# Optimization experiments

Hardware: AMD Instinct MI355X
Metric: run time of the kernel (lower is better)

Reference implementation:

```python
import jax, jax.numpy as jnp
import numpy as np

T, B, IN_DIM, HIDDEN = 512, 64, 512, 1024


def setup_inputs() -> dict:
    key = jax.random.key(0)
    k1, k2, k3, k4, k5 = jax.random.split(key, 5)
    x = jax.random.normal(k1, (T, B, IN_DIM), dtype=jnp.float32)
    h0 = jax.random.normal(k2, (B, HIDDEN), dtype=jnp.float32)
    # parameters initialized like torch.rand (uniform [0,1))
    Wx = jax.random.uniform(k3, (IN_DIM, HIDDEN), dtype=jnp.float32)
    Wh = jax.random.uniform(k4, (HIDDEN, HIDDEN), dtype=jnp.float32)
    b = jax.random.uniform(k5, (1, HIDDEN), dtype=jnp.float32)
    return {"x": x, "h0": h0, "Wx": Wx, "Wh": Wh, "b": b}


def reference(x, h0, Wx, Wh, b):
    # Precompute input projections for all timesteps in one big GEMM:
    # [T, B, in_dim] @ [in_dim, hidden] -> [T, B, hidden]
    xw = jnp.einsum('tbi,ih->tbh', x, Wx) + b  # bias fused here

    def step(h, xw_t):
        h = jnp.tanh(xw_t + h @ Wh)
        return h, h

    h_last, outs = jax.lax.scan(step, h0, xw)
    return outs, h_last
```

## Files before the change

kernel.cpp:

```cpp
#include <hip/hip_runtime.h>
#include <hip/hip_bf16.h>


#define T_ 512
#define B_ 64
#define IN_ 512
#define H_ 1024
constexpr int TBH = T_ * B_ * H_;
constexpr int HB  = B_ * H_;
constexpr int GP  = 1024 * 16;

typedef unsigned short u16;
typedef unsigned int u32;
typedef unsigned long long u64;
typedef __attribute__((ext_vector_type(8))) short short8;
typedef __attribute__((ext_vector_type(4))) float f32x4;

__device__ __forceinline__ void splitbf(float x, u16& hi, u16& lo) {
    unsigned u = __float_as_uint(x);
    hi = (u16)(u >> 16);
    float r = x - __uint_as_float(u & 0xffff0000u);
    lo = (u16)(__float_as_uint(r) >> 16);
}

__global__ void k_split4(const float4* __restrict__ in, u16* __restrict__ hi,
                         u16* __restrict__ lo, int n4) {
    int i = blockIdx.x * blockDim.x + threadIdx.x;
    int stride = gridDim.x * blockDim.x;
    for (; i < n4; i += stride) {
        float4 v = in[i];
        u16 h0,h1,h2,h3,l0,l1,l2,l3;
        splitbf(v.x,h0,l0); splitbf(v.y,h1,l1); splitbf(v.z,h2,l2); splitbf(v.w,h3,l3);
        uint2 hv, lv;
        hv.x = (unsigned)h0 | ((unsigned)h1 << 16);
        hv.y = (unsigned)h2 | ((unsigned)h3 << 16);
        lv.x = (unsigned)l0 | ((unsigned)l1 << 16);
        lv.y = (unsigned)l2 | ((unsigned)l3 << 16);
        *(uint2*)&hi[4*i] = hv;
        *(uint2*)&lo[4*i] = lv;
    }
}

__global__ void k_tsplit(const float* __restrict__ src, u16* __restrict__ hi,
                         u16* __restrict__ lo, int K, int N) {
    int id = blockIdx.x * 256 + threadIdx.x;
    if (id >= K * N) return;
    int k = id / N, n = id % N;
    u16 h, l; splitbf(src[id], h, l);
    hi[n*K + k] = h; lo[n*K + k] = l;
}

__global__ void k_h0(const float* __restrict__ h0, u32* __restrict__ hbufP) {
    int id = blockIdx.x * 256 + threadIdx.x;
    if (id >= HB) return;
    int b = id >> 10, k = id & 1023;
    u32 u = __float_as_uint(h0[id]);
    hbufP[(size_t)((b>>4)*2 + 1)*GP + k*16 + (b & 15)] = (u & 0xFFFFFF80u) | 127u;
}

__launch_bounds__(256, 2)
__global__ void k_gemm_xw(const u16* __restrict__ xhi, const u16* __restrict__ xlo,
                          const u16* __restrict__ wthi, const u16* __restrict__ wtlo,
                          const float* __restrict__ bias, float* __restrict__ out) {
    int bid = blockIdx.x;
    int mi = bid >> 3, ni = bid & 7;
    int m0 = mi * 128, n0 = ni * 128;
    int wave = threadIdx.x >> 6, lane = threadIdx.x & 63;
    int wr = wave >> 1, wc = wave & 1;
    int lrow = lane & 15, lk8 = (lane >> 4) * 8;
    const int rowb = m0 + wr*64 + lrow;
    const int colb = n0 + wc*64 + lrow;
    f32x4 acc[4][4] = {};
    for (int kt = 0; kt < 16; ++kt) {
        int kb = kt*32 + lk8;
        short8 ah[4], al[4], bh[4], bl[4];
#pragma unroll
        for (int mt = 0; mt < 4; ++mt) {
            ah[mt] = *(const short8*)&xhi[(size_t)(rowb + mt*16)*IN_ + kb];
            al[mt] = *(const short8*)&xlo[(size_t)(rowb + mt*16)*IN_ + kb];
        }
#pragma unroll
        for (int nt = 0; nt < 4; ++nt) {
            bh[nt] = *(const short8*)&wthi[(size_t)(colb + nt*16)*IN_ + kb];
            bl[nt] = *(const short8*)&wtlo[(size_t)(colb + nt*16)*IN_ + kb];
        }
#pragma unroll
        for (int mt = 0; mt < 4; ++mt)
#pragma unroll
            for (int nt = 0; nt < 4; ++nt) {
                acc[mt][nt] = __builtin_amdgcn_mfma_f32_16x16x32_bf16(ah[mt], bh[nt], acc[mt][nt], 0,0,0);
                acc[mt][nt] = __builtin_amdgcn_mfma_f32_16x16x32_bf16(ah[mt], bl[nt], acc[mt][nt], 0,0,0);
                acc[mt][nt] = __builtin_amdgcn_mfma_f32_16x16x32_bf16(al[mt], bh[nt], acc[mt][nt], 0,0,0);
            }
    }
    int orow0 = m0 + wr*64 + 4*(lane >> 4);
#pragma unroll
    for (int nt = 0; nt < 4; ++nt) {
        int col = n0 + wc*64 + nt*16 + (lane & 15);
        float bv = bias[col];
#pragma unroll
        for (int mt = 0; mt < 4; ++mt)
#pragma unroll
            for (int r = 0; r < 4; ++r)
                out[(size_t)(orow0 + mt*16 + r)*H_ + col] = acc[mt][nt][r] + bv;
    }
}

__global__ void k_gemm_f32(const float* __restrict__ A, const float* __restrict__ Bw,
                           const float* __restrict__ bias, float* __restrict__ out) {
    __shared__ float As[32][65];
    __shared__ float Bs[32][65];
    int n0 = blockIdx.x * 64, m0 = blockIdx.y * 64;
    int tid = threadIdx.x;
    int tr = tid >> 4, tc = tid & 15;
    float acc[4][4] = {};
    for (int kc = 0; kc < IN_; kc += 32) {
#pragma unroll
        for (int it = 0; it < 8; ++it) {
            int id = tid + 256*it;
            int k = id & 31, m = id >> 5;
            As[k][m] = A[(size_t)(m0 + m)*IN_ + kc + k];
        }
#pragma unroll
        for (int it = 0; it < 8; ++it) {
            int id = tid + 256*it;
            int n = id & 63, kk = id >> 6;
            Bs[kk][n] = Bw[(size_t)(kc + kk)*H_ + n0 + n];
        }
        __syncthreads();
#pragma unroll
        for (int kk = 0; kk < 32; ++kk) {
            float a[4], b[4];
#pragma unroll
            for (int i = 0; i < 4; ++i) a[i] = As[kk][tr*4+i];
#pragma unroll
            for (int j = 0; j < 4; ++j) b[j] = Bs[kk][tc*4+j];
#pragma unroll
            for (int i = 0; i < 4; ++i)
#pragma unroll
                for (int j = 0; j < 4; ++j) acc[i][j] += a[i]*b[j];
        }
        __syncthreads();
    }
#pragma unroll
    for (int i = 0; i < 4; ++i)
#pragma unroll
        for (int j = 0; j < 4; ++j)
            out[(size_t)(m0 + tr*4 + i)*H_ + n0 + tc*4 + j] = acc[i][j] + bias[n0 + tc*4 + j];
}

__launch_bounds__(512, 1)
__global__ void k_scan(const float* __restrict__ wh,
                       float* __restrict__ out,
                       u32* __restrict__ hbufP) {
    int bid = blockIdx.x;
    int g = bid >> 4, cw = bid & 15;
    int row_g = g * 16;
    int wave = threadIdx.x >> 6, lane = threadIdx.x & 63;
    int ks = wave & 3, ch = wave >> 2;
    int n0 = cw*64 + ch*32;
    int lrow = lane & 15, lk8 = (lane >> 4) * 8;
    __shared__ float partial[8 * 16 * 33];
    __shared__ float hx[16 * 1030];

    short8 bh[2][8], bl[2][8];
#pragma unroll
    for (int nt = 0; nt < 2; ++nt) {
        int col = n0 + nt*16 + lrow;
#pragma unroll
        for (int kt = 0; kt < 8; ++kt) {
            int kbase = ks*256 + kt*32 + lk8;
            short8 h8, l8;
#pragma unroll
            for (int j = 0; j < 8; ++j) {
                u16 hh, ll; splitbf(wh[(size_t)(kbase + j)*H_ + col], hh, ll);
                h8[j] = (short)hh; l8[j] = (short)ll;
            }
            bh[nt][kt] = h8; bl[nt][kt] = l8;
        }
    }

    const int ec  = threadIdx.x >> 3;
    const int er0 = (threadIdx.x & 7) * 2;
    const int ech = ec >> 5;
    const int ecl = ec & 31;

    float xw0 = out[(size_t)(row_g + er0    )*H_ + cw*64 + ec];
    float xw1 = out[(size_t)(row_g + er0 + 1)*H_ + cw*64 + ec];

    const int bcol = ks*256 + ch*128 + (lane >> 3);
    const int brow = 2 * (lane & 7);

    for (int t = 0; t < T_; ++t) {
        const u32 want = 64u | (u32)((t - 1) & 63);
        const u64 want64 = ((u64)want << 32) | (u64)want;
        const int par = t & 1;
        const u64* sb = (const u64*)(hbufP + (size_t)(g*2 + ((t+1)&1))*GP)
                        + ks*2048 + ch*1024;

        u64 raw[16];
        u32 pend = 0xFFFFu;
        for (;;) {
#pragma unroll
            for (int i = 0; i < 16; ++i)
                if (pend & (1u << i))
                    raw[i] = __hip_atomic_load(sb + i*64 + lane, __ATOMIC_RELAXED,
                                               __HIP_MEMORY_SCOPE_AGENT);
            u32 np = 0;
#pragma unroll
            for (int i = 0; i < 16; ++i)
                if (pend & (1u << i)) {
                    u64 bad = (raw[i] ^ want64) & 0x0000007F0000007FULL;
                    if (__any(bad != 0)) np |= 1u << i;
                }
            pend = np;
            if (pend == 0) break;
            __builtin_amdgcn_s_sleep(1);
        }
#pragma unroll
        for (int i = 0; i < 16; ++i) {
            int col = bcol + i*8;
            hx[brow*1030 + col]     = __uint_as_float((u32)raw[i]);
            hx[(brow+1)*1030 + col] = __uint_as_float((u32)(raw[i] >> 32));
        }
        __syncthreads();

        f32x4 acc[2][2] = {};
#pragma unroll
        for (int kt = 0; kt < 8; ++kt) {
            int p = kt & 1;
            short8 ah, al;
            int cb = lrow*1030 + ks*256 + kt*32 + lk8;
#pragma unroll
            for (int j = 0; j < 8; ++j) {
                u32 bits = __float_as_uint(hx[cb + j]);
                ah[j] = (short)(bits >> 16);
                float r = __uint_as_float(bits & 0xFFFFFF80u)
                        - __uint_as_float(bits & 0xFFFF0000u);
                al[j] = (short)(__float_as_uint(r) >> 16);
            }
#pragma unroll
            for (int nt = 0; nt < 2; ++nt) {
                acc[nt][p] = __builtin_amdgcn_mfma_f32_16x16x32_bf16(ah, bh[nt][kt], acc[nt][p], 0,0,0);
                acc[nt][p] = __builtin_amdgcn_mfma_f32_16x16x32_bf16(ah, bl[nt][kt], acc[nt][p], 0,0,0);
                acc[nt][p] = __builtin_amdgcn_mfma_f32_16x16x32_bf16(al, bh[nt][kt], acc[nt][p], 0,0,0);
            }
        }
        {
            int r0 = 4 * (lane >> 4);
#pragma unroll
            for (int nt = 0; nt < 2; ++nt) {
                int c = nt*16 + lrow;
#pragma unroll
                for (int r = 0; r < 4; ++r)
                    partial[((ch*4 + ks)*16 + r0 + r)*33 + c] = acc[nt][0][r] + acc[nt][1][r];
            }
        }
        __syncthreads();
        {
            float s0 = xw0, s1 = xw1;
#pragma unroll
            for (int w = 0; w < 4; ++w) {
                s0 += partial[((ech*4 + w)*16 + er0    )*33 + ecl];
                s1 += partial[((ech*4 + w)*16 + er0 + 1)*33 + ecl];
            }
            float y0 = tanhf(s0), y1 = tanhf(s1);
            const u32 tagt = 64u | (u32)(t & 63);
            u32 b0 = (__float_as_uint(y0) & 0xFFFFFF80u) | tagt;
            u32 b1 = (__float_as_uint(y1) & 0xFFFFFF80u) | tagt;
            u32* hnb = hbufP + (size_t)(g*2 + par)*GP + (cw*64 + ec)*16 + er0;
            (void)__hip_atomic_exchange((u64*)hnb, ((u64)b1 << 32) | (u64)b0,
                                        __ATOMIC_RELAXED, __HIP_MEMORY_SCOPE_AGENT);
            int gb0 = row_g + er0;
            out[(size_t)(t*B_ + gb0    )*H_ + cw*64 + ec] = y0;
            out[(size_t)(t*B_ + gb0 + 1)*H_ + cw*64 + ec] = y1;
            if (t == T_-1) {
                out[(size_t)TBH + (size_t)gb0*H_ + cw*64 + ec] = y0;
                out[(size_t)TBH + (size_t)(gb0+1)*H_ + cw*64 + ec] = y1;
            }
        }
        if (t + 1 < T_) {
            xw0 = out[(size_t)((t+1)*B_ + row_g + er0    )*H_ + cw*64 + ec];
            xw1 = out[(size_t)((t+1)*B_ + row_g + er0 + 1)*H_ + cw*64 + ec];
        }
    }
}

extern "C" void kernel_launch(void* const* d_in, const int* in_sizes, int n_in,
                              void* d_out, int out_size, void* d_ws, size_t ws_size,
                              hipStream_t stream) {
    const float* x    = (const float*)d_in[0];
    const float* h0   = (const float*)d_in[1];
    const float* Wx   = (const float*)d_in[2];
    const float* Wh   = (const float*)d_in[3];
    const float* bias = (const float*)d_in[4];
    float* out = (float*)d_out;

    const size_t nX = (size_t)T_ * B_ * IN_;
    const size_t nWx = (size_t)IN_ * H_;
    const size_t hbufB = (size_t)8 * GP * sizeof(u32);
    const size_t FULL_NEED = 2*nX*2 + 2*nWx*2 + hbufB;
    const size_t SAFE_NEED = hbufB;
    if (ws_size < SAFE_NEED) return;

    bool full = ws_size >= FULL_NEED;
    u16 *xhi = nullptr, *xlo = nullptr, *wthi = nullptr, *wtlo = nullptr;
    u32* hbufP;
    if (full) {
        xhi  = (u16*)d_ws;
        xlo  = xhi + nX;
        wthi = xlo + nX;
        wtlo = wthi + nWx;
        hbufP = (u32*)(wtlo + nWx);
    } else {
        hbufP = (u32*)d_ws;
    }

    hipMemsetAsync(hbufP, 0, hbufB, stream);
    k_h0<<<HB/256, 256, 0, stream>>>(h0, hbufP);
    if (full) {
        k_split4<<<2048, 256, 0, stream>>>((const float4*)x, xhi, xlo, (int)(nX/4));
        k_tsplit<<<(int)(nWx/256), 256, 0, stream>>>(Wx, wthi, wtlo, IN_, H_);
        k_gemm_xw<<<2048, 256, 0, stream>>>(xhi, xlo, wthi, wtlo, bias, out);
    } else {
        k_gemm_f32<<<dim3(16, 512), 256, 0, stream>>>(x, Wx, bias, out);
    }
    k_scan<<<64, 512, 0, stream>>>(Wh, out, hbufP);
}
```

Measured before the change: 2.401 ms.

## Split scan batch groups to 8 rows and prefetch next hidden state early

The recurrent scan kernel now gives each block 8 batch rows instead of 16, doubling the grid to 128 blocks. Per-step work and the global hidden-state exchange per block are halved, spreading the serial recurrence over more CUs. The next step's hidden-state loads are issued right after the MFMA stage, before the barrier and epilogue, and the poll loop sleeps only when no progress was made. The cost is half-empty MFMA tiles, since only 8 of 16 rows are used, idle epilogue threads, and more blocks taking part in the cross-block spin synchronisation.

```diff
diff --git a/kernel.cpp b/kernel.cpp
--- a/kernel.cpp
+++ b/kernel.cpp
@@ -8,7 +8,7 @@
 #define H_ 1024
 constexpr int TBH = T_ * B_ * H_;
 constexpr int HB  = B_ * H_;
-constexpr int GP  = 1024 * 16;
+constexpr int GP8 = 1024 * 8;
 
 typedef unsigned short u16;
 typedef unsigned int u32;
@@ -55,7 +55,7 @@
     if (id >= HB) return;
     int b = id >> 10, k = id & 1023;
     u32 u = __float_as_uint(h0[id]);
-    hbufP[(size_t)((b>>4)*2 + 1)*GP + k*16 + (b & 15)] = (u & 0xFFFFFF80u) | 127u;
+    hbufP[(size_t)((b>>3)*2 + 1)*GP8 + k*8 + (b & 7)] = (u & 0xFFFFFF80u) | 127u;
 }
 
 __launch_bounds__(256, 2)
@@ -155,13 +155,13 @@
                        u32* __restrict__ hbufP) {
     int bid = blockIdx.x;
     int g = bid >> 4, cw = bid & 15;
-    int row_g = g * 16;
+    int row_g = g * 8;
     int wave = threadIdx.x >> 6, lane = threadIdx.x & 63;
     int ks = wave & 3, ch = wave >> 2;
     int n0 = cw*64 + ch*32;
     int lrow = lane & 15, lk8 = (lane >> 4) * 8;
-    __shared__ float partial[8 * 16 * 33];
-    __shared__ float hx[16 * 1030];
+    __shared__ float partial[8 * 8 * 33];
+    __shared__ float hx[8 * 1030];
 
     short8 bh[2][8], bl[2][8];
 #pragma unroll
@@ -180,46 +180,58 @@
         }
     }
 
-    const int ec  = threadIdx.x >> 3;
-    const int er0 = (threadIdx.x & 7) * 2;
-    const int ech = ec >> 5;
+    const int ec  = threadIdx.x >> 2;
+    const int er0 = (threadIdx.x & 3) * 2;
+    const bool epi = (threadIdx.x < 256);
+    const int ech = (ec >> 5) & 1;
     const int ecl = ec & 31;
 
-    float xw0 = out[(size_t)(row_g + er0    )*H_ + cw*64 + ec];
-    float xw1 = out[(size_t)(row_g + er0 + 1)*H_ + cw*64 + ec];
-
-    const int bcol = ks*256 + ch*128 + (lane >> 3);
-    const int brow = 2 * (lane & 7);
+    float xw0 = 0.f, xw1 = 0.f;
+    if (epi) {
+        xw0 = out[(size_t)(row_g + er0    )*H_ + cw*64 + ec];
+        xw1 = out[(size_t)(row_g + er0 + 1)*H_ + cw*64 + ec];
+    }
+
+    const int bcol = wave*128 + (lane >> 2);
+    const int brow = 2 * (lane & 3);
+
+    u64 raw[8];
+    u32 pend = 0xFFu;
+    {
+        const u64* sb = (const u64*)(hbufP + (size_t)(g*2 + 1)*GP8) + wave*512;
+#pragma unroll
+        for (int i = 0; i < 8; ++i)
+            raw[i] = __hip_atomic_load(sb + i*64 + lane, __ATOMIC_RELAXED,
+                                       __HIP_MEMORY_SCOPE_AGENT);
+    }
 
     for (int t = 0; t < T_; ++t) {
         const u32 want = 64u | (u32)((t - 1) & 63);
         const u64 want64 = ((u64)want << 32) | (u64)want;
         const int par = t & 1;
-        const u64* sb = (const u64*)(hbufP + (size_t)(g*2 + ((t+1)&1))*GP)
-                        + ks*2048 + ch*1024;
-
-        u64 raw[16];
-        u32 pend = 0xFFFFu;
+        const u64* sb = (const u64*)(hbufP + (size_t)(g*2 + ((t+1)&1))*GP8) + wave*512;
+
         for (;;) {
-#pragma unroll
-            for (int i = 0; i < 16; ++i)
-                if (pend & (1u << i))
-                    raw[i] = __hip_atomic_load(sb + i*64 + lane, __ATOMIC_RELAXED,
-                                               __HIP_MEMORY_SCOPE_AGENT);
             u32 np = 0;
 #pragma unroll
-            for (int i = 0; i < 16; ++i)
+            for (int i = 0; i < 8; ++i)
                 if (pend & (1u << i)) {
                     u64 bad = (raw[i] ^ want64) & 0x0000007F0000007FULL;
                     if (__any(bad != 0)) np |= 1u << i;
                 }
+            u32 progress = pend ^ np;
             pend = np;
             if (pend == 0) break;
-            __builtin_amdgcn_s_sleep(1);
-        }
-#pragma unroll
-        for (int i = 0; i < 16; ++i) {
-            int col = bcol + i*8;
+            if (!progress) __builtin_amdgcn_s_sleep(1);
+#pragma unroll
+            for (int i = 0; i < 8; ++i)
+                if (pend & (1u << i))
+                    raw[i] = __hip_atomic_load(sb + i*64 + lane, __ATOMIC_RELAXED,
+                                               __HIP_MEMORY_SCOPE_AGENT);
+        }
+#pragma unroll
+        for (int i = 0; i < 8; ++i) {
+            int col = bcol + i*16;
             hx[brow*1030 + col]     = __uint_as_float((u32)raw[i]);
             hx[(brow+1)*1030 + col] = __uint_as_float((u32)(raw[i] >> 32));
         }
@@ -230,7 +242,7 @@
         for (int kt = 0; kt < 8; ++kt) {
             int p = kt & 1;
             short8 ah, al;
-            int cb = lrow*1030 + ks*256 + kt*32 + lk8;
+            int cb = (lrow & 7)*1030 + ks*256 + kt*32 + lk8;
 #pragma unroll
             for (int j = 0; j < 8; ++j) {
                 u32 bits = __float_as_uint(hx[cb + j]);
@@ -246,29 +258,39 @@
                 acc[nt][p] = __builtin_amdgcn_mfma_f32_16x16x32_bf16(al, bh[nt][kt], acc[nt][p], 0,0,0);
             }
         }
-        {
+        if (lane < 32) {
             int r0 = 4 * (lane >> 4);
 #pragma unroll
             for (int nt = 0; nt < 2; ++nt) {
                 int c = nt*16 + lrow;
 #pragma unroll
                 for (int r = 0; r < 4; ++r)
-                    partial[((ch*4 + ks)*16 + r0 + r)*33 + c] = acc[nt][0][r] + acc[nt][1][r];
-            }
-        }
+                    partial[((ch*4 + ks)*8 + r0 + r)*33 + c] = acc[nt][0][r] + acc[nt][1][r];
+            }
+        }
+
+        if (t + 1 < T_) {
+            const u64* sbn = (const u64*)(hbufP + (size_t)(g*2 + par)*GP8) + wave*512;
+#pragma unroll
+            for (int i = 0; i < 8; ++i)
+                raw[i] = __hip_atomic_load(sbn + i*64 + lane, __ATOMIC_RELAXED,
+                                           __HIP_MEMORY_SCOPE_AGENT);
+            pend = 0xFFu;
+        }
+
         __syncthreads();
-        {
+        if (epi) {
             float s0 = xw0, s1 = xw1;
 #pragma unroll
             for (int w = 0; w < 4; ++w) {
-                s0 += partial[((ech*4 + w)*16 + er0    )*33 + ecl];
-                s1 += partial[((ech*4 + w)*16 + er0 + 1)*33 + ecl];
+                s0 += partial[((ech*4 + w)*8 + er0    )*33 + ecl];
+                s1 += partial[((ech*4 + w)*8 + er0 + 1)*33 + ecl];
             }
             float y0 = tanhf(s0), y1 = tanhf(s1);
             const u32 tagt = 64u | (u32)(t & 63);
             u32 b0 = (__float_as_uint(y0) & 0xFFFFFF80u) | tagt;
             u32 b1 = (__float_as_uint(y1) & 0xFFFFFF80u) | tagt;
-            u32* hnb = hbufP + (size_t)(g*2 + par)*GP + (cw*64 + ec)*16 + er0;
+            u32* hnb = hbufP + (size_t)(g*2 + par)*GP8 + (cw*64 + ec)*8 + er0;
             (void)__hip_atomic_exchange((u64*)hnb, ((u64)b1 << 32) | (u64)b0,
                                         __ATOMIC_RELAXED, __HIP_MEMORY_SCOPE_AGENT);
             int gb0 = row_g + er0;
@@ -278,10 +300,10 @@
                 out[(size_t)TBH + (size_t)gb0*H_ + cw*64 + ec] = y0;
                 out[(size_t)TBH + (size_t)(gb0+1)*H_ + cw*64 + ec] = y1;
             }
-        }
-        if (t + 1 < T_) {
-            xw0 = out[(size_t)((t+1)*B_ + row_g + er0    )*H_ + cw*64 + ec];
-            xw1 = out[(size_t)((t+1)*B_ + row_g + er0 + 1)*H_ + cw*64 + ec];
+            if (t + 1 < T_) {
+                xw0 = out[(size_t)((t+1)*B_ + gb0    )*H_ + cw*64 + ec];
+                xw1 = out[(size_t)((t+1)*B_ + gb0 + 1)*H_ + cw*64 + ec];
+            }
         }
     }
 }
@@ -298,7 +320,7 @@
 
     const size_t nX = (size_t)T_ * B_ * IN_;
     const size_t nWx = (size_t)IN_ * H_;
-    const size_t hbufB = (size_t)8 * GP * sizeof(u32);
+    const size_t hbufB = (size_t)16 * GP8 * sizeof(u32);
     const size_t FULL_NEED = 2*nX*2 + 2*nWx*2 + hbufB;
     const size_t SAFE_NEED = hbufB;
     if (ws_size < SAFE_NEED) return;
@@ -325,5 +347,5 @@
     } else {
         k_gemm_f32<<<dim3(16, 512), 256, 0, stream>>>(x, Wx, bias, out);
     }
-    k_scan<<<64, 512, 0, stream>>>(Wh, out, hbufP);
-}
+    k_scan<<<128, 512, 0, stream>>>(Wh, out, hbufP);
+}
```

Measured after the change: 2.112 ms (median of 2 runs). 12.0% less time.
